# Performance work log

Hardware: AMD Instinct MI355X
Metric: run time of the kernel (lower is better)

## Reference

```python
import jax, jax.numpy as jnp
import numpy as np

FEATURES = 256
HIDDEN = 256
NUM_BINS = 10
NUM_BLOCKS = 2
MULT = 2 * NUM_BINS + 1  # tails=None -> widths(K) + heights(K+1)
MIN_BW = 1e-3
MIN_BH = 1e-3
BATCH = 8192


def _build_masks():
    # nflows MADE sequential degrees
    in_deg = np.arange(1, FEATURES + 1)
    hid_deg = np.arange(HIDDEN) % max(1, FEATURES - 1) + min(1, FEATURES - 1)
    m0 = (hid_deg[:, None] >= in_deg[None, :]).astype(np.float32)   # [H, F]
    mh = (hid_deg[:, None] >= hid_deg[None, :]).astype(np.float32)  # [H, H]
    out_deg = np.repeat(in_deg, MULT)                               # feature-major tiling (nflows _tile)
    mf = (out_deg[:, None] > hid_deg[None, :]).astype(np.float32)   # [F*MULT, H]
    return jnp.asarray(m0), jnp.asarray(mh), jnp.asarray(mf)

MASK0, MASKH, MASKF = _build_masks()


def setup_inputs() -> dict:
    key = jax.random.key(0)
    ks = jax.random.split(key, 7)
    s = 1.0 / np.sqrt(HIDDEN)
    return {
        "inputs": jax.random.uniform(ks[0], (BATCH, FEATURES), dtype=jnp.float32),
        "W0": jax.random.normal(ks[1], (HIDDEN, FEATURES), dtype=jnp.float32) * s,
        "b0": jax.random.normal(ks[2], (HIDDEN,), dtype=jnp.float32) * 0.01,
        "Wb": jax.random.normal(ks[3], (2 * NUM_BLOCKS, HIDDEN, HIDDEN), dtype=jnp.float32) * s,
        "bb": jax.random.normal(ks[4], (2 * NUM_BLOCKS, HIDDEN), dtype=jnp.float32) * 0.01,
        "Wf": jax.random.normal(ks[5], (FEATURES * MULT, HIDDEN), dtype=jnp.float32) * s,
        "bf": jax.random.normal(ks[6], (FEATURES * MULT,), dtype=jnp.float32) * 0.01,
    }


def _made(x, W0, b0, Wb, bb, Wf, bf):
    h = x @ (W0 * MASK0).T + b0
    for i in range(NUM_BLOCKS):  # pre-activation masked residual blocks
        t = jax.nn.relu(h)
        t = t @ (Wb[2 * i] * MASKH).T + bb[2 * i]
        t = jax.nn.relu(t)
        t = t @ (Wb[2 * i + 1] * MASKH).T + bb[2 * i + 1]
        h = h + t
    return h @ (Wf * MASKF).T + bf  # [B, F*MULT]


def _quadratic_spline(x, uw, uh):
    # x: [B,F]; uw: [B,F,K]; uh: [B,F,K+1]
    widths = jax.nn.softmax(uw, axis=-1)
    widths = MIN_BW + (1.0 - MIN_BW * NUM_BINS) * widths
    hexp = jnp.exp(uh)
    area = jnp.sum(0.5 * (hexp[..., :-1] + hexp[..., 1:]) * widths, axis=-1, keepdims=True)
    heights = hexp / area
    heights = MIN_BH + (1.0 - MIN_BH) * heights

    cdf = jnp.cumsum(0.5 * (heights[..., :-1] + heights[..., 1:]) * widths, axis=-1)
    cdf = cdf.at[..., -1].set(1.0)
    cdf = jnp.pad(cdf, [(0, 0), (0, 0), (1, 0)])
    locs = jnp.cumsum(widths, axis=-1)
    locs = locs.at[..., -1].set(1.0)
    locs = jnp.pad(locs, [(0, 0), (0, 0), (1, 0)])

    # searchsorted: sum(x >= knots) - 1, clamped into valid bins
    idx = jnp.clip(jnp.sum(x[..., None] >= locs, axis=-1) - 1, 0, NUM_BINS - 1)
    g = lambda t, i: jnp.take_along_axis(t, i[..., None], axis=-1)[..., 0]

    loc = g(locs, idx)
    w = g(widths, idx)
    lcdf = g(cdf, idx)
    hl = g(heights, idx)
    hr = g(heights, idx + 1)

    a = 0.5 * (hr - hl) * w
    b = hl * w
    alpha = (x - loc) / w
    out = jnp.clip(a * alpha * alpha + b * alpha + lcdf, 0.0, 1.0)
    logabsdet = jnp.log(alpha * (hr - hl) + hl)
    return out, jnp.sum(logabsdet, axis=-1)  # sum_except_batch


def reference(inputs, W0, b0, Wb, bb, Wf, bf):
    params = _made(inputs, W0, b0, Wb, bb, Wf, bf)
    tp = params.reshape(inputs.shape[0], FEATURES, MULT)
    scale = 1.0 / np.sqrt(HIDDEN).astype(np.float32)
    uw = tp[..., :NUM_BINS] * scale
    uh = tp[..., NUM_BINS:] * scale
    return _quadratic_spline(inputs, uw, uh)
```

## Files before the change

### kernel.cpp

```cpp
#include <hip/hip_runtime.h>

typedef _Float16 f16;
typedef f16 f16x8 __attribute__((ext_vector_type(8)));
typedef float f32x4 __attribute__((ext_vector_type(4)));

#define MFMA(A,B,C) __builtin_amdgcn_mfma_f32_16x16x32_f16(A,B,C,0,0,0)

#define PTRUNK 0u
#define PHEAD  655360u

#define SMEM_BYTES 80384

__device__ __forceinline__ void fsplit(float v, f16& hi, f16& lo) {
    hi = (f16)v;
    lo = (f16)(v - (float)hi);
}

__global__ __launch_bounds__(256) void prep_kernel(
    const float* __restrict__ W0, const float* __restrict__ Wb,
    const float* __restrict__ Wf, unsigned char* __restrict__ wsb)
{
    __shared__ f16 sm[16][264];
    const int b = blockIdx.x, t = threadIdx.x;
    const int cr = t >> 4, kc = t & 15;

    if (b < 80) {
        const int mat = b >> 4, ct = b & 15;
        const int c = ct * 16 + cr;
        const int cd = c % 255;
        const float* src = ((mat == 0) ? W0 : (Wb + (mat - 1) * 65536)) + c * 256;
        #pragma unroll
        for (int u = 0; u < 4; ++u) {
            const int k = kc * 16 + u * 4;
            float4 v = *(const float4*)(src + k);
            float vv[4] = {v.x, v.y, v.z, v.w};
            #pragma unroll
            for (int e = 0; e < 4; ++e) {
                int kk = k + e;
                int kd = (mat == 0) ? kk : (kk % 255);
                sm[cr][kk] = (cd >= kd) ? (f16)vv[e] : (f16)0.f;
            }
        }
        __syncthreads();
        const int ks = t >> 5, ln = t & 31;
        #pragma unroll
        for (int rep = 0; rep < 2; ++rep) {
            const int L = ln + rep * 32;
            const int li = L & 15, lg = L >> 4;
            f16x8 v = *(const f16x8*)&sm[li][ks * 32 + lg * 8];
            ((f16x8*)(wsb + PTRUNK))[(mat * 128 + ks * 16 + ct) * 64 + L] = v;
        }
    } else {
        const int hb = b - 80;
        const int bly = hb / 21, ct = hb - bly * 21;
        const int cl = ct * 16 + cr;
        const int fw = cl / 21;
        const int f  = bly * 16 + fw;
        const int m  = cl - fw * 21;
        const float* src = Wf + (f * 21 + m) * 256;
        #pragma unroll
        for (int u = 0; u < 4; ++u) {
            const int k = kc * 16 + u * 4;
            float4 v = *(const float4*)(src + k);
            float vv[4] = {v.x, v.y, v.z, v.w};
            #pragma unroll
            for (int e = 0; e < 4; ++e) {
                int kk = k + e;
                int jd = kk % 255;
                sm[cr][(kk + 1) & 255] = (f > jd) ? (f16)vv[e] : (f16)0.f;
            }
        }
        __syncthreads();
        const int ks = t >> 5, ln = t & 31;
        #pragma unroll
        for (int rep = 0; rep < 2; ++rep) {
            const int L = ln + rep * 32;
            const int li = L & 15, lg = L >> 4;
            f16x8 v = *(const f16x8*)&sm[li][ks * 32 + lg * 8];
            ((f16x8*)(wsb + PHEAD))[((bly * 8 + ks) * 21 + ct) * 64 + L] = v;
        }
    }
}

__global__ __launch_bounds__(512, 2) void mega_kernel(
    const float* __restrict__ x, const unsigned char* __restrict__ wsb,
    const float* __restrict__ b0, const float* __restrict__ bb,
    const float* __restrict__ bfp, float* __restrict__ out,
    float* __restrict__ lad)
{
    extern __shared__ unsigned char smem[];
    f16 (*Ah1)[264] = (f16(*)[264])(smem);
    f16 (*Al1)[264] = (f16(*)[264])(smem + 16896);
    f16 (*Ah0)[264] = (f16(*)[264])(smem + 33792);
    f16 (*Al0)[264] = (f16(*)[264])(smem + 50688);
    float* prm      = (float*)(smem + 33792);
    float* ladp     = (float*)(smem + 79360);

    const int t = threadIdx.x, lane = t & 63;
    const int wu = __builtin_amdgcn_readfirstlane(t >> 6);
    const int li = lane & 15, lg = lane >> 4;
    const int r0 = blockIdx.x * 32;

    {
        const int row = t >> 4, cb = (t & 15) * 16;
        const float* xr = x + (r0 + row) * 256 + cb;
        f16 hi[16], lo[16];
        #pragma unroll
        for (int j = 0; j < 16; j += 4) {
            float4 v4 = *(const float4*)(xr + j);
            fsplit(v4.x, hi[j],     lo[j]);
            fsplit(v4.y, hi[j + 1], lo[j + 1]);
            fsplit(v4.z, hi[j + 2], lo[j + 2]);
            fsplit(v4.w, hi[j + 3], lo[j + 3]);
        }
        *(f16x8*)&Ah0[row][cb]     = *(f16x8*)&hi[0];
        *(f16x8*)&Ah0[row][cb + 8] = *(f16x8*)&hi[8];
        *(f16x8*)&Al0[row][cb]     = *(f16x8*)&lo[0];
        *(f16x8*)&Al0[row][cb + 8] = *(f16x8*)&lo[8];
    }
    __syncthreads();

    const f16x8* wt = (const f16x8*)(wsb + PTRUNK);
    const f16x8* wh = (const f16x8*)(wsb + PHEAD);

    const int ctA = wu, ctB = 15 - wu;
    const int nkA = (ctA >> 1) + 1;
    const int nkB = (ctB >> 1) + 1;

    f32x4 acc[2][2], h[2][2];

    auto gemm = [&](int mat, f16 (*Sh)[264], f16 (*Sl)[264],
                    const float* __restrict__ bias) {
        const int a7 = (mat > 0) ? 1 : 0;
        const int tB = nkB + ((a7 && nkB < 8) ? 1 : 0);
        const f16x8* wb = wt + mat * 8192;
        f16x8 bfA[9], bfB[9];
        #pragma unroll
        for (int s = 0; s < 9; ++s) {
            if (s < tB) {
                const int ks = (s < nkB) ? s : 7;
                bfB[s] = wb[(ks * 16 + ctB) * 64 + lane];
                if (ks < nkA || (a7 && ks == 7))
                    bfA[s] = wb[(ks * 16 + ctA) * 64 + lane];
            }
        }
        #pragma unroll
        for (int ci = 0; ci < 2; ++ci)
            #pragma unroll
            for (int rt = 0; rt < 2; ++rt)
                acc[ci][rt] = (f32x4){0.f, 0.f, 0.f, 0.f};
        #pragma unroll
        for (int s = 0; s < 9; ++s) {
            if (s < tB) {
                const int ks = (s < nkB) ? s : 7;
                const int ko = ks * 32 + lg * 8;
                f16x8 ah0 = *(const f16x8*)&Sh[li][ko];
                f16x8 al0 = *(const f16x8*)&Sl[li][ko];
                f16x8 ah1 = *(const f16x8*)&Sh[16 + li][ko];
                f16x8 al1 = *(const f16x8*)&Sl[16 + li][ko];
                acc[1][0] = MFMA(al0, bfB[s], acc[1][0]);
                acc[1][0] = MFMA(ah0, bfB[s], acc[1][0]);
                acc[1][1] = MFMA(al1, bfB[s], acc[1][1]);
                acc[1][1] = MFMA(ah1, bfB[s], acc[1][1]);
                if (ks < nkA || (a7 && ks == 7)) {
                    acc[0][0] = MFMA(al0, bfA[s], acc[0][0]);
                    acc[0][0] = MFMA(ah0, bfA[s], acc[0][0]);
                    acc[0][1] = MFMA(al1, bfA[s], acc[0][1]);
                    acc[0][1] = MFMA(ah1, bfA[s], acc[0][1]);
                }
            }
        }
        const float bvA = bias[ctA * 16 + li];
        const float bvB = bias[ctB * 16 + li];
        #pragma unroll
        for (int rt = 0; rt < 2; ++rt)
            #pragma unroll
            for (int q = 0; q < 4; ++q) {
                acc[0][rt][q] += bvA;
                acc[1][rt][q] += bvB;
            }
    };

    auto store_act = [&](f16 (*Dh)[264], f16 (*Dl)[264], f32x4 (&s)[2][2],
                         bool relu, bool rot) {
        #pragma unroll
        for (int ci = 0; ci < 2; ++ci) {
            const int c  = (ci ? ctB : ctA) * 16 + li;
            const int cc = rot ? ((c + 1) & 255) : c;
            #pragma unroll
            for (int rt = 0; rt < 2; ++rt)
                #pragma unroll
                for (int q = 0; q < 4; ++q) {
                    float v = s[ci][rt][q];
                    if (relu) v = fmaxf(v, 0.f);
                    f16 hi, lo; fsplit(v, hi, lo);
                    Dh[rt * 16 + lg * 4 + q][cc] = hi;
                    Dl[rt * 16 + lg * 4 + q][cc] = lo;
                }
        }
    };

    gemm(0, Ah0, Al0, b0);
    #pragma unroll
    for (int ci = 0; ci < 2; ++ci)
        #pragma unroll
        for (int rt = 0; rt < 2; ++rt) h[ci][rt] = acc[ci][rt];
    store_act(Ah1, Al1, acc, true, false);
    __syncthreads();

    gemm(1, Ah1, Al1, bb);
    store_act(Ah0, Al0, acc, true, false);
    __syncthreads();

    gemm(2, Ah0, Al0, bb + 256);
    #pragma unroll
    for (int ci = 0; ci < 2; ++ci)
        #pragma unroll
        for (int rt = 0; rt < 2; ++rt) h[ci][rt] += acc[ci][rt];
    store_act(Ah1, Al1, h, true, false);
    __syncthreads();

    gemm(3, Ah1, Al1, bb + 512);
    store_act(Ah0, Al0, acc, true, false);
    __syncthreads();

    gemm(4, Ah0, Al0, bb + 768);
    #pragma unroll
    for (int ci = 0; ci < 2; ++ci)
        #pragma unroll
        for (int rt = 0; rt < 2; ++rt) h[ci][rt] += acc[ci][rt];
    store_act(Ah1, Al1, h, false, true);
    __syncthreads();

    float lr0 = 0.f, lr1 = 0.f;

    auto do_half = [&](const f32x4* hacc, int hp, float xv, int pass, int f0,
                       int fme, float& lr) {
        #pragma unroll
        for (int ci = 0; ci < 6; ++ci) {
            const int cl = (pass * 5 + ci) * 16 + li;
            const int fw = cl / 21;
            const int m  = cl - fw * 21;
            if (fw >= pass * 4 && fw < pass * 4 + 4) {
                const float bv = bfp[f0 * 21 + cl];
                #pragma unroll
                for (int q = 0; q < 4; ++q)
                    prm[(wu * 16 + lg * 4 + q) * 89 + (fw - pass * 4) * 22 + m] =
                        (hacc[ci][q] + bv) * 0.0625f;
            }
        }
        float p[21];
        #pragma unroll
        for (int m = 0; m < 21; ++m)
            p[m] = prm[(wu * 16 + li) * 89 + lg * 22 + m];

        float wmax = p[0];
        #pragma unroll
        for (int i = 1; i < 10; ++i) wmax = fmaxf(wmax, p[i]);
        float ew[10]; float wsum = 0.f;
        #pragma unroll
        for (int i = 0; i < 10; ++i) { ew[i] = __expf(p[i] - wmax); wsum += ew[i]; }
        const float winv = 1.0f / wsum;
        float wid[10];
        #pragma unroll
        for (int i = 0; i < 10; ++i) wid[i] = 1.0e-3f + 0.99f * ew[i] * winv;

        float hx[11];
        #pragma unroll
        for (int i = 0; i < 11; ++i) hx[i] = __expf(p[10 + i]);
        float area = 0.f;
        #pragma unroll
        for (int i = 0; i < 10; ++i) area += (hx[i] + hx[i + 1]) * wid[i];
        const float ainv = 2.0f / area;
        float hts[11];
        #pragma unroll
        for (int i = 0; i < 11; ++i) hts[i] = 1.0e-3f + 0.999f * hx[i] * ainv;

        float la = wid[0];
        float ca = 0.5f * (hts[0] + hts[1]) * wid[0];
        float loc = 0.f, ww = wid[0], lc = 0.f, hl = hts[0], hr = hts[1];
        #pragma unroll
        for (int i = 1; i < 10; ++i) {
            const bool sel = (xv >= la);
            loc = sel ? la : loc;
            ww  = sel ? wid[i] : ww;
            lc  = sel ? ca : lc;
            hl  = sel ? hts[i] : hl;
            hr  = sel ? hts[i + 1] : hr;
            la += wid[i];
            ca += 0.5f * (hts[i] + hts[i + 1]) * wid[i];
        }
        const float al2 = (xv - loc) / ww;
        const float dh  = hr - hl;
        float y = (0.5f * dh * ww * al2 + hl * ww) * al2 + lc;
        y = fminf(fmaxf(y, 0.f), 1.f);
        out[(r0 + hp * 16 + li) * 256 + fme] = y;
        lr += __logf(al2 * dh + hl);
    };

    #pragma unroll
    for (int ib = 0; ib < 2; ++ib) {
        const int bly = ib ? (15 - wu) : wu;
        const int nl  = (bly + 2) >> 1;
        const int f0  = bly * 16;
        const int bly8 = bly * 8;

        #pragma unroll
        for (int pass = 0; pass < 4; ++pass) {
            const int p5  = pass * 5;
            const int fme = f0 + pass * 4 + lg;
            const float xv0 = x[(r0 + li) * 256 + fme];
            const float xv1 = x[(r0 + 16 + li) * 256 + fme];

            f32x4 pA[6], pB[6];
            #pragma unroll
            for (int ci = 0; ci < 6; ++ci) {
                pA[ci] = (f32x4){0.f, 0.f, 0.f, 0.f};
                pB[ci] = (f32x4){0.f, 0.f, 0.f, 0.f};
            }

            f16x8 c0[6], c1[6];
            #pragma unroll
            for (int ci = 0; ci < 6; ++ci)
                c0[ci] = wh[(bly8 * 21 + p5 + ci) * 64 + lane];

            __builtin_amdgcn_s_setprio(1);
            for (int s = 0; s < nl; s += 2) {
                const int s1 = (s + 1 < nl) ? s + 1 : 0;
                #pragma unroll
                for (int ci = 0; ci < 6; ++ci)
                    c1[ci] = wh[((bly8 + s1) * 21 + p5 + ci) * 64 + lane];
                {
                    const int ko = s * 32 + lg * 8;
                    f16x8 ah0 = *(const f16x8*)&Ah1[li][ko];
                    f16x8 al0 = *(const f16x8*)&Al1[li][ko];
                    f16x8 ah1 = *(const f16x8*)&Ah1[16 + li][ko];
                    f16x8 al1 = *(const f16x8*)&Al1[16 + li][ko];
                    #pragma unroll
                    for (int ci = 0; ci < 6; ++ci) {
                        pA[ci] = MFMA(al0, c0[ci], pA[ci]);
                        pA[ci] = MFMA(ah0, c0[ci], pA[ci]);
                        pB[ci] = MFMA(al1, c0[ci], pB[ci]);
                        pB[ci] = MFMA(ah1, c0[ci], pB[ci]);
                    }
                }
                const int s2 = (s + 2 < nl) ? s + 2 : 0;
                #pragma unroll
                for (int ci = 0; ci < 6; ++ci)
                    c0[ci] = wh[((bly8 + s2) * 21 + p5 + ci) * 64 + lane];
                if (s + 1 < nl) {
                    const int ko = s1 * 32 + lg * 8;
                    f16x8 ah0 = *(const f16x8*)&Ah1[li][ko];
                    f16x8 al0 = *(const f16x8*)&Al1[li][ko];
                    f16x8 ah1 = *(const f16x8*)&Ah1[16 + li][ko];
                    f16x8 al1 = *(const f16x8*)&Al1[16 + li][ko];
                    #pragma unroll
                    for (int ci = 0; ci < 6; ++ci) {
                        pA[ci] = MFMA(al0, c1[ci], pA[ci]);
                        pA[ci] = MFMA(ah0, c1[ci], pA[ci]);
                        pB[ci] = MFMA(al1, c1[ci], pB[ci]);
                        pB[ci] = MFMA(ah1, c1[ci], pB[ci]);
                    }
                }
            }
            __builtin_amdgcn_s_setprio(0);

            do_half(pA, 0, xv0, pass, f0, fme, lr0);
            do_half(pB, 1, xv1, pass, f0, fme, lr1);
        }
    }

    lr0 += __shfl_xor(lr0, 16); lr0 += __shfl_xor(lr0, 32);
    lr1 += __shfl_xor(lr1, 16); lr1 += __shfl_xor(lr1, 32);
    if (lane < 16) {
        ladp[wu * 32 + lane]      = lr0;
        ladp[wu * 32 + 16 + lane] = lr1;
    }
    __syncthreads();
    if (t < 32) {
        float s = 0.f;
        #pragma unroll
        for (int w2 = 0; w2 < 8; ++w2) s += ladp[w2 * 32 + t];
        lad[r0 + t] = s;
    }
}

extern "C" void kernel_launch(void* const* d_in, const int* in_sizes, int n_in,
                              void* d_out, int out_size, void* d_ws, size_t ws_size,
                              hipStream_t stream)
{
    const float* x  = (const float*)d_in[0];
    const float* W0 = (const float*)d_in[1];
    const float* b0 = (const float*)d_in[2];
    const float* Wb = (const float*)d_in[3];
    const float* bb = (const float*)d_in[4];
    const float* Wf = (const float*)d_in[5];
    const float* bf = (const float*)d_in[6];

    float* out = (float*)d_out;
    float* lad = out + 8192 * 256;
    unsigned char* wsb = (unsigned char*)d_ws;

    hipFuncSetAttribute(reinterpret_cast<const void*>(mega_kernel),
                        hipFuncAttributeMaxDynamicSharedMemorySize, SMEM_BYTES);

    prep_kernel<<<416, 256, 0, stream>>>(W0, Wb, Wf, wsb);
    mega_kernel<<<256, 512, SMEM_BYTES, stream>>>(x, wsb, b0, bb, bf, out, lad);
}
```

Measured before the change: 136.9 us.

## Fuse weight-prep kernel into main kernel via cooperative grid sync

Moves the masked fp16 weight packing from a separate prep kernel into the start of the main kernel. Each block packs two 16-row tiles using half the shared memory per tile, then a grid-wide cooperative sync waits before the MLP and spline work begins. This removes one kernel launch and the gap between the two kernels. In exchange it adds a grid barrier, a cooperative launch path, and the requirement that all 256 blocks be resident at once.

Measured after the change: 189.4 us. 38.4% more time.

```diff
diff --git a/kernel.cpp b/kernel.cpp
--- a/kernel.cpp
+++ b/kernel.cpp
@@ -1,4 +1,5 @@
 #include <hip/hip_runtime.h>
+#include <hip/hip_cooperative_groups.h>
 
 typedef _Float16 f16;
 typedef f16 f16x8 __attribute__((ext_vector_type(8)));
@@ -16,77 +17,12 @@
     lo = (f16)(v - (float)hi);
 }
 
-__global__ __launch_bounds__(256) void prep_kernel(
-    const float* __restrict__ W0, const float* __restrict__ Wb,
-    const float* __restrict__ Wf, unsigned char* __restrict__ wsb)
-{
-    __shared__ f16 sm[16][264];
-    const int b = blockIdx.x, t = threadIdx.x;
-    const int cr = t >> 4, kc = t & 15;
-
-    if (b < 80) {
-        const int mat = b >> 4, ct = b & 15;
-        const int c = ct * 16 + cr;
-        const int cd = c % 255;
-        const float* src = ((mat == 0) ? W0 : (Wb + (mat - 1) * 65536)) + c * 256;
-        #pragma unroll
-        for (int u = 0; u < 4; ++u) {
-            const int k = kc * 16 + u * 4;
-            float4 v = *(const float4*)(src + k);
-            float vv[4] = {v.x, v.y, v.z, v.w};
-            #pragma unroll
-            for (int e = 0; e < 4; ++e) {
-                int kk = k + e;
-                int kd = (mat == 0) ? kk : (kk % 255);
-                sm[cr][kk] = (cd >= kd) ? (f16)vv[e] : (f16)0.f;
-            }
-        }
-        __syncthreads();
-        const int ks = t >> 5, ln = t & 31;
-        #pragma unroll
-        for (int rep = 0; rep < 2; ++rep) {
-            const int L = ln + rep * 32;
-            const int li = L & 15, lg = L >> 4;
-            f16x8 v = *(const f16x8*)&sm[li][ks * 32 + lg * 8];
-            ((f16x8*)(wsb + PTRUNK))[(mat * 128 + ks * 16 + ct) * 64 + L] = v;
-        }
-    } else {
-        const int hb = b - 80;
-        const int bly = hb / 21, ct = hb - bly * 21;
-        const int cl = ct * 16 + cr;
-        const int fw = cl / 21;
-        const int f  = bly * 16 + fw;
-        const int m  = cl - fw * 21;
-        const float* src = Wf + (f * 21 + m) * 256;
-        #pragma unroll
-        for (int u = 0; u < 4; ++u) {
-            const int k = kc * 16 + u * 4;
-            float4 v = *(const float4*)(src + k);
-            float vv[4] = {v.x, v.y, v.z, v.w};
-            #pragma unroll
-            for (int e = 0; e < 4; ++e) {
-                int kk = k + e;
-                int jd = kk % 255;
-                sm[cr][(kk + 1) & 255] = (f > jd) ? (f16)vv[e] : (f16)0.f;
-            }
-        }
-        __syncthreads();
-        const int ks = t >> 5, ln = t & 31;
-        #pragma unroll
-        for (int rep = 0; rep < 2; ++rep) {
-            const int L = ln + rep * 32;
-            const int li = L & 15, lg = L >> 4;
-            f16x8 v = *(const f16x8*)&sm[li][ks * 32 + lg * 8];
-            ((f16x8*)(wsb + PHEAD))[((bly * 8 + ks) * 21 + ct) * 64 + L] = v;
-        }
-    }
-}
-
 __global__ __launch_bounds__(512, 2) void mega_kernel(
-    const float* __restrict__ x, const unsigned char* __restrict__ wsb,
-    const float* __restrict__ b0, const float* __restrict__ bb,
-    const float* __restrict__ bfp, float* __restrict__ out,
-    float* __restrict__ lad)
+    const float* __restrict__ x, unsigned char* __restrict__ wsb,
+    const float* __restrict__ W0, const float* __restrict__ b0,
+    const float* __restrict__ Wb, const float* __restrict__ bb,
+    const float* __restrict__ Wf, const float* __restrict__ bfp,
+    float* __restrict__ out, float* __restrict__ lad)
 {
     extern __shared__ unsigned char smem[];
     f16 (*Ah1)[264] = (f16(*)[264])(smem);
@@ -100,6 +36,72 @@
     const int wu = __builtin_amdgcn_readfirstlane(t >> 6);
     const int li = lane & 15, lg = lane >> 4;
     const int r0 = blockIdx.x * 32;
+
+    {
+        f16 (*sm)[264] = (f16(*)[264])(smem + (t >> 8) * 8448);
+        const int tl = t & 255;
+        const int cr = tl >> 4, kc = tl & 15;
+        const int u  = blockIdx.x * 2 + (t >> 8);
+
+        if (u < 80) {
+            const int mat = u >> 4, ct = u & 15;
+            const int c = ct * 16 + cr;
+            const int cd = c % 255;
+            const float* src = ((mat == 0) ? W0 : (Wb + (mat - 1) * 65536)) + c * 256;
+            #pragma unroll
+            for (int uu = 0; uu < 4; ++uu) {
+                const int k = kc * 16 + uu * 4;
+                float4 v = *(const float4*)(src + k);
+                float vv[4] = {v.x, v.y, v.z, v.w};
+                #pragma unroll
+                for (int e = 0; e < 4; ++e) {
+                    int kk = k + e;
+                    int kd = (mat == 0) ? kk : (kk % 255);
+                    sm[cr][kk] = (cd >= kd) ? (f16)vv[e] : (f16)0.f;
+                }
+            }
+        } else if (u < 416) {
+            const int hb = u - 80;
+            const int bly = hb / 21, ct = hb - bly * 21;
+            const int cl = ct * 16 + cr;
+            const int fw = cl / 21;
+            const int f  = bly * 16 + fw;
+            const int m  = cl - fw * 21;
+            const float* src = Wf + (f * 21 + m) * 256;
+            #pragma unroll
+            for (int uu = 0; uu < 4; ++uu) {
+                const int k = kc * 16 + uu * 4;
+                float4 v = *(const float4*)(src + k);
+                float vv[4] = {v.x, v.y, v.z, v.w};
+                #pragma unroll
+                for (int e = 0; e < 4; ++e) {
+                    int kk = k + e;
+                    int jd = kk % 255;
+                    sm[cr][(kk + 1) & 255] = (f > jd) ? (f16)vv[e] : (f16)0.f;
+                }
+            }
+        }
+        __syncthreads();
+        if (u < 416) {
+            const int ks = tl >> 5, ln = tl & 31;
+            #pragma unroll
+            for (int rep = 0; rep < 2; ++rep) {
+                const int L  = ln + rep * 32;
+                const int l2 = L & 15, g2 = L >> 4;
+                f16x8 v = *(const f16x8*)&sm[l2][ks * 32 + g2 * 8];
+                if (u < 80) {
+                    const int mat = u >> 4, ct = u & 15;
+                    ((f16x8*)(wsb + PTRUNK))[(mat * 128 + ks * 16 + ct) * 64 + L] = v;
+                } else {
+                    const int hb = u - 80;
+                    const int bly = hb / 21, ct = hb - bly * 21;
+                    ((f16x8*)(wsb + PHEAD))[((bly * 8 + ks) * 21 + ct) * 64 + L] = v;
+                }
+            }
+        }
+        cooperative_groups::this_grid().sync();
+    }
+
 
     {
         const int row = t >> 4, cb = (t & 15) * 16;
@@ -404,6 +406,9 @@
     hipFuncSetAttribute(reinterpret_cast<const void*>(mega_kernel),
                         hipFuncAttributeMaxDynamicSharedMemorySize, SMEM_BYTES);
 
-    prep_kernel<<<416, 256, 0, stream>>>(W0, Wb, Wf, wsb);
-    mega_kernel<<<256, 512, SMEM_BYTES, stream>>>(x, wsb, b0, bb, bf, out, lad);
+    void* args[] = {(void*)&x, (void*)&wsb, (void*)&W0, (void*)&b0,
+                    (void*)&Wb, (void*)&bb, (void*)&Wf, (void*)&bf,
+                    (void*)&out, (void*)&lad};
+    hipLaunchCooperativeKernel(reinterpret_cast<void*>(mega_kernel),
+                               dim3(256), dim3(512), args, SMEM_BYTES, stream);
 }
```

## Halve rows per block to 16 and double grid for occupancy

Applied to the files above, without the earlier changes.

Each workgroup now processes 16 batch rows instead of 32, which halves the activation LDS buffers and the MFMA accumulators, and the grid grows from 256 to 512 blocks. Launch bounds request 4 blocks per CU so the 256 CUs can each hold more resident workgroups. The cost is that every weight fragment loaded from global memory now feeds only one 16-row tile instead of two, doubling weight traffic per row processed.

Measured after the change: 137.8 us. About the same (+0.6%).

```diff
diff --git a/kernel.cpp b/kernel.cpp
--- a/kernel.cpp
+++ b/kernel.cpp
@@ -9,7 +9,7 @@
 #define PTRUNK 0u
 #define PHEAD  655360u
 
-#define SMEM_BYTES 80384
+#define SMEM_BYTES 62976
 
 __device__ __forceinline__ void fsplit(float v, f16& hi, f16& lo) {
     hi = (f16)v;
@@ -82,7 +82,7 @@
     }
 }
 
-__global__ __launch_bounds__(512, 2) void mega_kernel(
+__global__ __launch_bounds__(512, 4) void mega_kernel(
     const float* __restrict__ x, const unsigned char* __restrict__ wsb,
     const float* __restrict__ b0, const float* __restrict__ bb,
     const float* __restrict__ bfp, float* __restrict__ out,
@@ -90,33 +90,28 @@
 {
     extern __shared__ unsigned char smem[];
     f16 (*Ah1)[264] = (f16(*)[264])(smem);
-    f16 (*Al1)[264] = (f16(*)[264])(smem + 16896);
-    f16 (*Ah0)[264] = (f16(*)[264])(smem + 33792);
-    f16 (*Al0)[264] = (f16(*)[264])(smem + 50688);
-    float* prm      = (float*)(smem + 33792);
-    float* ladp     = (float*)(smem + 79360);
+    f16 (*Al1)[264] = (f16(*)[264])(smem + 8448);
+    f16 (*Ah0)[264] = (f16(*)[264])(smem + 16896);
+    f16 (*Al0)[264] = (f16(*)[264])(smem + 25344);
+    float* prm      = (float*)(smem + 16896);
+    float* ladp     = (float*)(smem + 62464);
 
     const int t = threadIdx.x, lane = t & 63;
     const int wu = __builtin_amdgcn_readfirstlane(t >> 6);
     const int li = lane & 15, lg = lane >> 4;
-    const int r0 = blockIdx.x * 32;
+    const int r0 = blockIdx.x * 16;
 
     {
-        const int row = t >> 4, cb = (t & 15) * 16;
+        const int row = t >> 5, cb = (t & 31) * 8;
         const float* xr = x + (r0 + row) * 256 + cb;
-        f16 hi[16], lo[16];
-        #pragma unroll
-        for (int j = 0; j < 16; j += 4) {
-            float4 v4 = *(const float4*)(xr + j);
-            fsplit(v4.x, hi[j],     lo[j]);
-            fsplit(v4.y, hi[j + 1], lo[j + 1]);
-            fsplit(v4.z, hi[j + 2], lo[j + 2]);
-            fsplit(v4.w, hi[j + 3], lo[j + 3]);
-        }
-        *(f16x8*)&Ah0[row][cb]     = *(f16x8*)&hi[0];
-        *(f16x8*)&Ah0[row][cb + 8] = *(f16x8*)&hi[8];
-        *(f16x8*)&Al0[row][cb]     = *(f16x8*)&lo[0];
-        *(f16x8*)&Al0[row][cb + 8] = *(f16x8*)&lo[8];
+        float4 va = *(const float4*)(xr);
+        float4 vb = *(const float4*)(xr + 4);
+        float v[8] = {va.x, va.y, va.z, va.w, vb.x, vb.y, vb.z, vb.w};
+        f16 hi[8], lo[8];
+        #pragma unroll
+        for (int j = 0; j < 8; ++j) fsplit(v[j], hi[j], lo[j]);
+        *(f16x8*)&Ah0[row][cb] = *(f16x8*)hi;
+        *(f16x8*)&Al0[row][cb] = *(f16x8*)lo;
     }
     __syncthreads();
 
@@ -127,7 +122,7 @@
     const int nkA = (ctA >> 1) + 1;
     const int nkB = (ctB >> 1) + 1;
 
-    f32x4 acc[2][2], h[2][2];
+    f32x4 acc[2], h[2];
 
     auto gemm = [&](int mat, f16 (*Sh)[264], f16 (*Sl)[264],
                     const float* __restrict__ bias) {
@@ -144,67 +139,48 @@
                     bfA[s] = wb[(ks * 16 + ctA) * 64 + lane];
             }
         }
-        #pragma unroll
-        for (int ci = 0; ci < 2; ++ci)
-            #pragma unroll
-            for (int rt = 0; rt < 2; ++rt)
-                acc[ci][rt] = (f32x4){0.f, 0.f, 0.f, 0.f};
+        acc[0] = (f32x4){0.f, 0.f, 0.f, 0.f};
+        acc[1] = (f32x4){0.f, 0.f, 0.f, 0.f};
         #pragma unroll
         for (int s = 0; s < 9; ++s) {
             if (s < tB) {
                 const int ks = (s < nkB) ? s : 7;
                 const int ko = ks * 32 + lg * 8;
-                f16x8 ah0 = *(const f16x8*)&Sh[li][ko];
-                f16x8 al0 = *(const f16x8*)&Sl[li][ko];
-                f16x8 ah1 = *(const f16x8*)&Sh[16 + li][ko];
-                f16x8 al1 = *(const f16x8*)&Sl[16 + li][ko];
-                acc[1][0] = MFMA(al0, bfB[s], acc[1][0]);
-                acc[1][0] = MFMA(ah0, bfB[s], acc[1][0]);
-                acc[1][1] = MFMA(al1, bfB[s], acc[1][1]);
-                acc[1][1] = MFMA(ah1, bfB[s], acc[1][1]);
+                f16x8 ah = *(const f16x8*)&Sh[li][ko];
+                f16x8 al = *(const f16x8*)&Sl[li][ko];
+                acc[1] = MFMA(al, bfB[s], acc[1]);
+                acc[1] = MFMA(ah, bfB[s], acc[1]);
                 if (ks < nkA || (a7 && ks == 7)) {
-                    acc[0][0] = MFMA(al0, bfA[s], acc[0][0]);
-                    acc[0][0] = MFMA(ah0, bfA[s], acc[0][0]);
-                    acc[0][1] = MFMA(al1, bfA[s], acc[0][1]);
-                    acc[0][1] = MFMA(ah1, bfA[s], acc[0][1]);
+                    acc[0] = MFMA(al, bfA[s], acc[0]);
+                    acc[0] = MFMA(ah, bfA[s], acc[0]);
                 }
             }
         }
         const float bvA = bias[ctA * 16 + li];
         const float bvB = bias[ctB * 16 + li];
         #pragma unroll
-        for (int rt = 0; rt < 2; ++rt)
-            #pragma unroll
-            for (int q = 0; q < 4; ++q) {
-                acc[0][rt][q] += bvA;
-                acc[1][rt][q] += bvB;
-            }
+        for (int q = 0; q < 4; ++q) { acc[0][q] += bvA; acc[1][q] += bvB; }
     };
 
-    auto store_act = [&](f16 (*Dh)[264], f16 (*Dl)[264], f32x4 (&s)[2][2],
+    auto store_act = [&](f16 (*Dh)[264], f16 (*Dl)[264], f32x4 (&s)[2],
                          bool relu, bool rot) {
         #pragma unroll
         for (int ci = 0; ci < 2; ++ci) {
             const int c  = (ci ? ctB : ctA) * 16 + li;
             const int cc = rot ? ((c + 1) & 255) : c;
             #pragma unroll
-            for (int rt = 0; rt < 2; ++rt)
-                #pragma unroll
-                for (int q = 0; q < 4; ++q) {
-                    float v = s[ci][rt][q];
-                    if (relu) v = fmaxf(v, 0.f);
-                    f16 hi, lo; fsplit(v, hi, lo);
-                    Dh[rt * 16 + lg * 4 + q][cc] = hi;
-                    Dl[rt * 16 + lg * 4 + q][cc] = lo;
-                }
+            for (int q = 0; q < 4; ++q) {
+                float v = s[ci][q];
+                if (relu) v = fmaxf(v, 0.f);
+                f16 hi, lo; fsplit(v, hi, lo);
+                Dh[lg * 4 + q][cc] = hi;
+                Dl[lg * 4 + q][cc] = lo;
+            }
         }
     };
 
     gemm(0, Ah0, Al0, b0);
-    #pragma unroll
-    for (int ci = 0; ci < 2; ++ci)
-        #pragma unroll
-        for (int rt = 0; rt < 2; ++rt) h[ci][rt] = acc[ci][rt];
+    h[0] = acc[0]; h[1] = acc[1];
     store_act(Ah1, Al1, acc, true, false);
     __syncthreads();
 
@@ -213,10 +189,7 @@
     __syncthreads();
 
     gemm(2, Ah0, Al0, bb + 256);
-    #pragma unroll
-    for (int ci = 0; ci < 2; ++ci)
-        #pragma unroll
-        for (int rt = 0; rt < 2; ++rt) h[ci][rt] += acc[ci][rt];
+    h[0] += acc[0]; h[1] += acc[1];
     store_act(Ah1, Al1, h, true, false);
     __syncthreads();
 
@@ -225,16 +198,13 @@
     __syncthreads();
 
     gemm(4, Ah0, Al0, bb + 768);
-    #pragma unroll
-    for (int ci = 0; ci < 2; ++ci)
-        #pragma unroll
-        for (int rt = 0; rt < 2; ++rt) h[ci][rt] += acc[ci][rt];
+    h[0] += acc[0]; h[1] += acc[1];
     store_act(Ah1, Al1, h, false, true);
     __syncthreads();
 
-    float lr0 = 0.f, lr1 = 0.f;
-
-    auto do_half = [&](const f32x4* hacc, int hp, float xv, int pass, int f0,
+    float lr0 = 0.f;
+
+    auto do_half = [&](const f32x4* hacc, float xv, int pass, int f0,
                        int fme, float& lr) {
         #pragma unroll
         for (int ci = 0; ci < 6; ++ci) {
@@ -294,7 +264,7 @@
         const float dh  = hr - hl;
         float y = (0.5f * dh * ww * al2 + hl * ww) * al2 + lc;
         y = fminf(fmaxf(y, 0.f), 1.f);
-        out[(r0 + hp * 16 + li) * 256 + fme] = y;
+        out[(r0 + li) * 256 + fme] = y;
         lr += __logf(al2 * dh + hl);
     };
 
@@ -310,14 +280,10 @@
             const int p5  = pass * 5;
             const int fme = f0 + pass * 4 + lg;
             const float xv0 = x[(r0 + li) * 256 + fme];
-            const float xv1 = x[(r0 + 16 + li) * 256 + fme];
-
-            f32x4 pA[6], pB[6];
-            #pragma unroll
-            for (int ci = 0; ci < 6; ++ci) {
-                pA[ci] = (f32x4){0.f, 0.f, 0.f, 0.f};
-                pB[ci] = (f32x4){0.f, 0.f, 0.f, 0.f};
-            }
+
+            f32x4 pA[6];
+            #pragma unroll
+            for (int ci = 0; ci < 6; ++ci) pA[ci] = (f32x4){0.f, 0.f, 0.f, 0.f};
 
             f16x8 c0[6], c1[6];
             #pragma unroll
@@ -332,16 +298,12 @@
                     c1[ci] = wh[((bly8 + s1) * 21 + p5 + ci) * 64 + lane];
                 {
                     const int ko = s * 32 + lg * 8;
-                    f16x8 ah0 = *(const f16x8*)&Ah1[li][ko];
-                    f16x8 al0 = *(const f16x8*)&Al1[li][ko];
-                    f16x8 ah1 = *(const f16x8*)&Ah1[16 + li][ko];
-                    f16x8 al1 = *(const f16x8*)&Al1[16 + li][ko];
+                    f16x8 ah = *(const f16x8*)&Ah1[li][ko];
+                    f16x8 al = *(const f16x8*)&Al1[li][ko];
                     #pragma unroll
                     for (int ci = 0; ci < 6; ++ci) {
-                        pA[ci] = MFMA(al0, c0[ci], pA[ci]);
-                        pA[ci] = MFMA(ah0, c0[ci], pA[ci]);
-                        pB[ci] = MFMA(al1, c0[ci], pB[ci]);
-                        pB[ci] = MFMA(ah1, c0[ci], pB[ci]);
+                        pA[ci] = MFMA(al, c0[ci], pA[ci]);
+                        pA[ci] = MFMA(ah, c0[ci], pA[ci]);
                     }
                 }
                 const int s2 = (s + 2 < nl) ? s + 2 : 0;
@@ -350,37 +312,29 @@
                     c0[ci] = wh[((bly8 + s2) * 21 + p5 + ci) * 64 + lane];
                 if (s + 1 < nl) {
                     const int ko = s1 * 32 + lg * 8;
-                    f16x8 ah0 = *(const f16x8*)&Ah1[li][ko];
-                    f16x8 al0 = *(const f16x8*)&Al1[li][ko];
-                    f16x8 ah1 = *(const f16x8*)&Ah1[16 + li][ko];
-                    f16x8 al1 = *(const f16x8*)&Al1[16 + li][ko];
+                    f16x8 ah = *(const f16x8*)&Ah1[li][ko];
+                    f16x8 al = *(const f16x8*)&Al1[li][ko];
                     #pragma unroll
                     for (int ci = 0; ci < 6; ++ci) {
-                        pA[ci] = MFMA(al0, c1[ci], pA[ci]);
-                        pA[ci] = MFMA(ah0, c1[ci], pA[ci]);
-                        pB[ci] = MFMA(al1, c1[ci], pB[ci]);
-                        pB[ci] = MFMA(ah1, c1[ci], pB[ci]);
+                        pA[ci] = MFMA(al, c1[ci], pA[ci]);
+                        pA[ci] = MFMA(ah, c1[ci], pA[ci]);
                     }
                 }
             }
             __builtin_amdgcn_s_setprio(0);
 
-            do_half(pA, 0, xv0, pass, f0, fme, lr0);
-            do_half(pB, 1, xv1, pass, f0, fme, lr1);
+            do_half(pA, xv0, pass, f0, fme, lr0);
         }
     }
 
-    lr0 += __shfl_xor(lr0, 16); lr0 += __shfl_xor(lr0, 32);
-    lr1 += __shfl_xor(lr1, 16); lr1 += __shfl_xor(lr1, 32);
-    if (lane < 16) {
-        ladp[wu * 32 + lane]      = lr0;
-        ladp[wu * 32 + 16 + lane] = lr1;
-    }
-    __syncthreads();
-    if (t < 32) {
+    lr0 += __shfl_xor(lr0, 16);
+    lr0 += __shfl_xor(lr0, 32);
+    if (lane < 16) ladp[wu * 16 + lane] = lr0;
+    __syncthreads();
+    if (t < 16) {
         float s = 0.f;
         #pragma unroll
-        for (int w2 = 0; w2 < 8; ++w2) s += ladp[w2 * 32 + t];
+        for (int w2 = 0; w2 < 8; ++w2) s += ladp[w2 * 16 + t];
         lad[r0 + t] = s;
     }
 }
@@ -405,5 +359,5 @@
                         hipFuncAttributeMaxDynamicSharedMemorySize, SMEM_BYTES);
 
     prep_kernel<<<416, 256, 0, stream>>>(W0, Wb, Wf, wsb);
-    mega_kernel<<<256, 512, SMEM_BYTES, stream>>>(x, wsb, b0, bb, bf, out, lad);
+    mega_kernel<<<512, 512, SMEM_BYTES, stream>>>(x, wsb, b0, bb, bf, out, lad);
 }
```

## Deepen head GEMM weight prefetch to four stages and pad activation pitch

Applied to the files above, without the earlier changes.

Replaces the two-stage register double buffer for head weight fragments with a four-stage rotating prefetch, so global loads are issued further ahead of the MFMAs that consume them. Separately, the shared-memory row pitch for activations grows from 264 to 272 halves to change the LDS bank mapping. The deeper prefetch uses many more VGPRs (four sets of six f16x8), which under launch_bounds(512,2) risks spills. The loop also now issues redundant loads for stages past the end, and the padding slightly enlarges LDS use.

Result: no change. 138.3 us (+1.0%).

```diff
diff --git a/kernel.cpp b/kernel.cpp
--- a/kernel.cpp
+++ b/kernel.cpp
@@ -9,7 +9,8 @@
 #define PTRUNK 0u
 #define PHEAD  655360u
 
-#define SMEM_BYTES 80384
+#define SMEM_BYTES 81408
+#define APITCH 272
 
 __device__ __forceinline__ void fsplit(float v, f16& hi, f16& lo) {
     hi = (f16)v;
@@ -89,12 +90,12 @@
     float* __restrict__ lad)
 {
     extern __shared__ unsigned char smem[];
-    f16 (*Ah1)[264] = (f16(*)[264])(smem);
-    f16 (*Al1)[264] = (f16(*)[264])(smem + 16896);
-    f16 (*Ah0)[264] = (f16(*)[264])(smem + 33792);
-    f16 (*Al0)[264] = (f16(*)[264])(smem + 50688);
-    float* prm      = (float*)(smem + 33792);
-    float* ladp     = (float*)(smem + 79360);
+    f16 (*Ah1)[APITCH] = (f16(*)[APITCH])(smem);
+    f16 (*Al1)[APITCH] = (f16(*)[APITCH])(smem + 17408);
+    f16 (*Ah0)[APITCH] = (f16(*)[APITCH])(smem + 34816);
+    f16 (*Al0)[APITCH] = (f16(*)[APITCH])(smem + 52224);
+    float* prm         = (float*)(smem + 34816);
+    float* ladp        = (float*)(smem + 80384);
 
     const int t = threadIdx.x, lane = t & 63;
     const int wu = __builtin_amdgcn_readfirstlane(t >> 6);
@@ -129,7 +130,7 @@
 
     f32x4 acc[2][2], h[2][2];
 
-    auto gemm = [&](int mat, f16 (*Sh)[264], f16 (*Sl)[264],
+    auto gemm = [&](int mat, f16 (*Sh)[APITCH], f16 (*Sl)[APITCH],
                     const float* __restrict__ bias) {
         const int a7 = (mat > 0) ? 1 : 0;
         const int tB = nkB + ((a7 && nkB < 8) ? 1 : 0);
@@ -181,7 +182,7 @@
             }
     };
 
-    auto store_act = [&](f16 (*Dh)[264], f16 (*Dl)[264], f32x4 (&s)[2][2],
+    auto store_act = [&](f16 (*Dh)[APITCH], f16 (*Dl)[APITCH], f32x4 (&s)[2][2],
                          bool relu, bool rot) {
         #pragma unroll
         for (int ci = 0; ci < 2; ++ci) {
@@ -319,49 +320,36 @@
                 pB[ci] = (f32x4){0.f, 0.f, 0.f, 0.f};
             }
 
-            f16x8 c0[6], c1[6];
-            #pragma unroll
-            for (int ci = 0; ci < 6; ++ci)
-                c0[ci] = wh[(bly8 * 21 + p5 + ci) * 64 + lane];
-
-            __builtin_amdgcn_s_setprio(1);
-            for (int s = 0; s < nl; s += 2) {
-                const int s1 = (s + 1 < nl) ? s + 1 : 0;
+            f16x8 c0[6], c1[6], c2[6], c3[6];
+            auto LD = [&](f16x8* dst, int s) {
+                const int ss = (s < nl) ? s : 0;
                 #pragma unroll
                 for (int ci = 0; ci < 6; ++ci)
-                    c1[ci] = wh[((bly8 + s1) * 21 + p5 + ci) * 64 + lane];
-                {
-                    const int ko = s * 32 + lg * 8;
-                    f16x8 ah0 = *(const f16x8*)&Ah1[li][ko];
-                    f16x8 al0 = *(const f16x8*)&Al1[li][ko];
-                    f16x8 ah1 = *(const f16x8*)&Ah1[16 + li][ko];
-                    f16x8 al1 = *(const f16x8*)&Al1[16 + li][ko];
-                    #pragma unroll
-                    for (int ci = 0; ci < 6; ++ci) {
-                        pA[ci] = MFMA(al0, c0[ci], pA[ci]);
-                        pA[ci] = MFMA(ah0, c0[ci], pA[ci]);
-                        pB[ci] = MFMA(al1, c0[ci], pB[ci]);
-                        pB[ci] = MFMA(ah1, c0[ci], pB[ci]);
-                    }
+                    dst[ci] = wh[((bly8 + ss) * 21 + p5 + ci) * 64 + lane];
+            };
+            auto COMP = [&](const f16x8* c, int s) {
+                const int ko = s * 32 + lg * 8;
+                f16x8 ah0 = *(const f16x8*)&Ah1[li][ko];
+                f16x8 al0 = *(const f16x8*)&Al1[li][ko];
+                f16x8 ah1 = *(const f16x8*)&Ah1[16 + li][ko];
+                f16x8 al1 = *(const f16x8*)&Al1[16 + li][ko];
+                #pragma unroll
+                for (int ci = 0; ci < 6; ++ci) {
+                    pA[ci] = MFMA(al0, c[ci], pA[ci]);
+                    pA[ci] = MFMA(ah0, c[ci], pA[ci]);
+                    pB[ci] = MFMA(al1, c[ci], pB[ci]);
+                    pB[ci] = MFMA(ah1, c[ci], pB[ci]);
                 }
-                const int s2 = (s + 2 < nl) ? s + 2 : 0;
-                #pragma unroll
-                for (int ci = 0; ci < 6; ++ci)
-                    c0[ci] = wh[((bly8 + s2) * 21 + p5 + ci) * 64 + lane];
-                if (s + 1 < nl) {
-                    const int ko = s1 * 32 + lg * 8;
-                    f16x8 ah0 = *(const f16x8*)&Ah1[li][ko];
-                    f16x8 al0 = *(const f16x8*)&Al1[li][ko];
-                    f16x8 ah1 = *(const f16x8*)&Ah1[16 + li][ko];
-                    f16x8 al1 = *(const f16x8*)&Al1[16 + li][ko];
-                    #pragma unroll
-                    for (int ci = 0; ci < 6; ++ci) {
-                        pA[ci] = MFMA(al0, c1[ci], pA[ci]);
-                        pA[ci] = MFMA(ah0, c1[ci], pA[ci]);
-                        pB[ci] = MFMA(al1, c1[ci], pB[ci]);
-                        pB[ci] = MFMA(ah1, c1[ci], pB[ci]);
-                    }
-                }
+            };
+
+            LD(c0, 0); LD(c1, 1); LD(c2, 2); LD(c3, 3);
+
+            __builtin_amdgcn_s_setprio(1);
+            for (int s = 0; s < nl; s += 4) {
+                COMP(c0, s); LD(c0, s + 4);
+                if (s + 1 < nl) { COMP(c1, s + 1); LD(c1, s + 5); }
+                if (s + 2 < nl) { COMP(c2, s + 2); LD(c2, s + 6); }
+                if (s + 3 < nl) { COMP(c3, s + 3); LD(c3, s + 7); }
             }
             __builtin_amdgcn_s_setprio(0);
 
```
